# Optimization experiments

Hardware: AMD Instinct MI355X
Metric: run time of the kernel (lower is better)

The kernel has to match this reference:

```python
import jax, jax.numpy as jnp
import numpy as np

BETA = 0.95
THR = 1.0  # snntorch Leaky default threshold

# Heaviside spike with ATan surrogate gradient (snntorch default, alpha=2):
# d/dx = 1 / (1 + (pi*x)^2)
@jax.custom_vjp
def spike_fn(x):
    return (x > 0).astype(x.dtype)

def _spike_fwd(x):
    return spike_fn(x), x

def _spike_bwd(x, g):
    return (g / (1.0 + (jnp.pi * x) ** 2),)

spike_fn.defvjp(_spike_fwd, _spike_bwd)


def setup_inputs() -> dict:
    key = jax.random.key(0)
    ks = jax.random.split(key, 5)
    T, B, D_in, D_h, D_out = 25, 4096, 784, 1000, 10
    x = jax.random.normal(ks[0], (T, B, D_in), dtype=jnp.float32)
    # Kaiming-uniform-ish init like nn.Linear
    w1 = jax.random.uniform(ks[1], (D_h, D_in), jnp.float32, -1, 1) / np.sqrt(D_in)
    b1 = jax.random.uniform(ks[2], (D_h,), jnp.float32, -1, 1) / np.sqrt(D_in)
    w2 = jax.random.uniform(ks[3], (D_out, D_h), jnp.float32, -1, 1) / np.sqrt(D_h)
    b2 = jax.random.uniform(ks[4], (D_out,), jnp.float32, -1, 1) / np.sqrt(D_h)
    return {"x": x, "w1": w1, "b1": b1, "w2": w2, "b2": b2}


def reference(x, w1, b1, w2, b2):
    B = x.shape[1]
    mem1_0 = jnp.zeros((B, w1.shape[0]), x.dtype)
    mem2_0 = jnp.zeros((B, w2.shape[0]), x.dtype)

    def step(carry, xt):
        mem1, mem2 = carry
        # layer 1: Linear + Leaky (reset-by-subtraction, reset from prior mem)
        cur1 = xt @ w1.T + b1
        reset1 = spike_fn(mem1 - THR)
        mem1 = BETA * mem1 + cur1 - reset1 * THR
        spk1 = spike_fn(mem1 - THR)
        # layer 2
        cur2 = spk1 @ w2.T + b2
        reset2 = spike_fn(mem2 - THR)
        mem2 = BETA * mem2 + cur2 - reset2 * THR
        spk2 = spike_fn(mem2 - THR)
        return (mem1, mem2), spk2

    (mem1, mem2), spk_rec = jax.lax.scan(step, (mem1_0, mem2_0), x)
    return spk_rec, mem2
```

## Files before the change

### kernel.cpp

```cpp
#include <hip/hip_runtime.h>

typedef _Float16 f16;
typedef _Float16 f16x4 __attribute__((ext_vector_type(4)));
typedef _Float16 f16x8 __attribute__((ext_vector_type(8)));
typedef float f32x4 __attribute__((ext_vector_type(4)));

#define T_STEPS 25
#define BATCH   4096
#define DIN     784
#define DH      1000
#define HP      1024
#define DOUT    10
#define MROWS   (T_STEPS * BATCH)
#define KSEG    800
#define KA      (2 * KSEG)
#define KB      (3 * KSEG)
#define NTILES  (KB / 32)

__global__ void aconv_kernel(const float* __restrict__ x, f16* __restrict__ Ah)
{
    const int total = MROWS * 200;
    for (int idx = blockIdx.x * blockDim.x + threadIdx.x; idx < total;
         idx += gridDim.x * blockDim.x) {
        const int r  = idx / 200;
        const int c4 = (idx - r * 200) * 4;
        f16x4 hi, lo;
        if (c4 < DIN) {
            const float4 v = *(const float4*)(x + (size_t)r * DIN + c4);
            const float vv[4] = {v.x, v.y, v.z, v.w};
            #pragma unroll
            for (int j = 0; j < 4; ++j) {
                f16 h = (f16)vv[j];
                hi[j] = h;
                lo[j] = (f16)(vv[j] - (float)h);
            }
        } else {
            #pragma unroll
            for (int j = 0; j < 4; ++j) { hi[j] = (f16)0.f; lo[j] = (f16)0.f; }
        }
        *(f16x4*)(Ah + (size_t)r * KA + c4)        = hi;
        *(f16x4*)(Ah + (size_t)r * KA + KSEG + c4) = lo;
    }
}

__global__ void wconv_kernel(const float* __restrict__ w1, const float* __restrict__ b1,
                             const float* __restrict__ w2,
                             f16* __restrict__ Wh, float* __restrict__ b1p,
                             float* __restrict__ w2t)
{
    const int stride = gridDim.x * blockDim.x;
    const int tid0 = blockIdx.x * blockDim.x + threadIdx.x;
    for (int idx = tid0; idx < HP * KB; idx += stride) {
        const int n  = idx / KB;
        const int k  = idx - n * KB;
        const int seg = k / KSEG;
        const int kc  = k - seg * KSEG;
        float w = (n < DH && kc < DIN) ? w1[n * DIN + kc] : 0.f;
        f16 h = (f16)w;
        Wh[idx] = (seg < 2) ? h : (f16)(w - (float)h);
    }
    for (int idx = tid0; idx < HP; idx += stride)
        b1p[idx] = (idx < DH) ? b1[idx] : 0.f;
    for (int idx = tid0; idx < HP * DOUT; idx += stride) {
        const int h = idx / DOUT;
        const int o = idx - h * DOUT;
        w2t[idx] = (h < DH) ? w2[o * DH + h] : 0.f;
    }
}

#define GL(gp, ldsoff) __builtin_amdgcn_global_load_lds( \
    (const __attribute__((address_space(1))) void*)(gp), \
    (__attribute__((address_space(3))) void*)(lds + (ldsoff)), 16, 0, 0)

#define STAGE_A(tt) do { \
    const int ak_ = (((tt) < 50) ? (tt) : ((tt) - 50)) * 32; \
    GL(Ag + ak_,            ((tt) & 3) * 8192 + widoff); \
    GL(Ag + ak_ + 128 * KA, ((tt) & 3) * 8192 + 4096 + widoff); } while (0)
#define STAGE_B(tt) do { \
    const int bk_ = (tt) * 32; \
    GL(Bg + bk_,                     32768 + ((tt) & 3) * 8192 + widoff); \
    GL(Bg + bk_ + (size_t)128 * KB,  32768 + ((tt) & 3) * 8192 + 4096 + widoff); } while (0)

#define MFMA16(M0) \
    acc[M0+0][0] = __builtin_amdgcn_mfma_f32_16x16x32_f16(af0, bf0, acc[M0+0][0], 0, 0, 0); \
    acc[M0+0][1] = __builtin_amdgcn_mfma_f32_16x16x32_f16(af0, bf1, acc[M0+0][1], 0, 0, 0); \
    acc[M0+0][2] = __builtin_amdgcn_mfma_f32_16x16x32_f16(af0, bf2, acc[M0+0][2], 0, 0, 0); \
    acc[M0+0][3] = __builtin_amdgcn_mfma_f32_16x16x32_f16(af0, bf3, acc[M0+0][3], 0, 0, 0); \
    acc[M0+1][0] = __builtin_amdgcn_mfma_f32_16x16x32_f16(af1, bf0, acc[M0+1][0], 0, 0, 0); \
    acc[M0+1][1] = __builtin_amdgcn_mfma_f32_16x16x32_f16(af1, bf1, acc[M0+1][1], 0, 0, 0); \
    acc[M0+1][2] = __builtin_amdgcn_mfma_f32_16x16x32_f16(af1, bf2, acc[M0+1][2], 0, 0, 0); \
    acc[M0+1][3] = __builtin_amdgcn_mfma_f32_16x16x32_f16(af1, bf3, acc[M0+1][3], 0, 0, 0); \
    acc[M0+2][0] = __builtin_amdgcn_mfma_f32_16x16x32_f16(af2, bf0, acc[M0+2][0], 0, 0, 0); \
    acc[M0+2][1] = __builtin_amdgcn_mfma_f32_16x16x32_f16(af2, bf1, acc[M0+2][1], 0, 0, 0); \
    acc[M0+2][2] = __builtin_amdgcn_mfma_f32_16x16x32_f16(af2, bf2, acc[M0+2][2], 0, 0, 0); \
    acc[M0+2][3] = __builtin_amdgcn_mfma_f32_16x16x32_f16(af2, bf3, acc[M0+2][3], 0, 0, 0); \
    acc[M0+3][0] = __builtin_amdgcn_mfma_f32_16x16x32_f16(af3, bf0, acc[M0+3][0], 0, 0, 0); \
    acc[M0+3][1] = __builtin_amdgcn_mfma_f32_16x16x32_f16(af3, bf1, acc[M0+3][1], 0, 0, 0); \
    acc[M0+3][2] = __builtin_amdgcn_mfma_f32_16x16x32_f16(af3, bf2, acc[M0+3][2], 0, 0, 0); \
    acc[M0+3][3] = __builtin_amdgcn_mfma_f32_16x16x32_f16(af3, bf3, acc[M0+3][3], 0, 0, 0);

#define BODY(tt, STG, WAITSTR) do { \
    const int bA = ((tt) & 3) * 8192; \
    const int bB = 32768 + ((tt) & 3) * 8192; \
    f16x8 af0, af1, af2, af3, bf0, bf1, bf2, bf3; \
     \
    af0 = *(const f16x8*)(lds + bA + aoffb + 0 * 512); \
    af1 = *(const f16x8*)(lds + bA + aoffb + 1 * 512); \
    af2 = *(const f16x8*)(lds + bA + aoffb + 2 * 512); \
    af3 = *(const f16x8*)(lds + bA + aoffb + 3 * 512); \
    bf0 = *(const f16x8*)(lds + bB + boffb + 0 * 512); \
    bf1 = *(const f16x8*)(lds + bB + boffb + 1 * 512); \
    bf2 = *(const f16x8*)(lds + bB + boffb + 2 * 512); \
    bf3 = *(const f16x8*)(lds + bB + boffb + 3 * 512); \
    if (STG) STAGE_A((tt) + 3); \
    __builtin_amdgcn_s_barrier(); \
    asm volatile("s_waitcnt lgkmcnt(0)" ::: "memory"); \
    __builtin_amdgcn_sched_barrier(0); \
    __builtin_amdgcn_s_setprio(1); \
    MFMA16(0) \
    __builtin_amdgcn_s_setprio(0); \
    __builtin_amdgcn_s_barrier(); \
     \
    af0 = *(const f16x8*)(lds + bA + aoffb + 4 * 512); \
    af1 = *(const f16x8*)(lds + bA + aoffb + 5 * 512); \
    af2 = *(const f16x8*)(lds + bA + aoffb + 6 * 512); \
    af3 = *(const f16x8*)(lds + bA + aoffb + 7 * 512); \
    if (STG) STAGE_B((tt) + 3); \
    asm volatile(WAITSTR ::: "memory"); \
    __builtin_amdgcn_s_barrier(); \
    asm volatile("s_waitcnt lgkmcnt(0)" ::: "memory"); \
    __builtin_amdgcn_sched_barrier(0); \
    __builtin_amdgcn_s_setprio(1); \
    MFMA16(4) \
    __builtin_amdgcn_s_setprio(0); \
    __builtin_amdgcn_s_barrier(); \
} while (0)

__global__ __launch_bounds__(512, 2)
void gemm_kernel(const f16* __restrict__ A, const f16* __restrict__ B,
                 const float* __restrict__ bias, float* __restrict__ C)
{
    __shared__ f16 lds[65536];

    const int bid = blockIdx.x;
    const int swz = (bid & 7) * 200 + (bid >> 3);
    const int mt = swz >> 2;
    const int nt = swz & 3;
    const size_t rowBase = (size_t)mt * 256;
    const int colBase = nt * 256;

    const int tid  = threadIdx.x;
    const int wid  = tid >> 6;
    const int lane = tid & 63;
    const int wm = wid >> 2;
    const int wn = wid & 3;

    const int srow = tid >> 2;
    const int g = (tid & 3) ^ ((tid >> 3) & 3);
    const f16* Ag = A + (rowBase + srow) * KA + g * 8;
    const f16* Bg = B + (size_t)(colBase + srow) * KB + g * 8;
    const int widoff = wid * 512;

    const int cq = (lane >> 4) ^ (((lane & 15) >> 1) & 3);
    const int aoffb = (wm * 128 + (lane & 15)) * 32 + cq * 8;
    const int boffb = (wn * 64  + (lane & 15)) * 32 + cq * 8;

    f32x4 acc[8][4];
    #pragma unroll
    for (int m = 0; m < 8; ++m)
        #pragma unroll
        for (int n = 0; n < 4; ++n)
            acc[m][n] = (f32x4){0.f, 0.f, 0.f, 0.f};

    STAGE_A(0 - 3 + 3); STAGE_B(0);
    STAGE_A(1);         STAGE_B(1);
    STAGE_A(2);         STAGE_B(2);
    asm volatile("s_waitcnt vmcnt(8)" ::: "memory");
    __builtin_amdgcn_s_barrier();

    #pragma unroll 4
    for (int t = 0; t < NTILES - 3; ++t)
        BODY(t, 1, "s_waitcnt vmcnt(8)");
    BODY(NTILES - 3, 0, "s_waitcnt vmcnt(4)");
    BODY(NTILES - 2, 0, "s_waitcnt vmcnt(0)");
    BODY(NTILES - 1, 0, "");

    const int c_col0 = colBase + wn * 64 + (lane & 15);
    const size_t c_row0 = rowBase + wm * 128 + (lane >> 4) * 4;
    #pragma unroll
    for (int n = 0; n < 4; ++n) {
        const int gcol = c_col0 + n * 16;
        const float bv = bias[gcol];
        #pragma unroll
        for (int m = 0; m < 8; ++m) {
            const size_t grow = c_row0 + m * 16;
            #pragma unroll
            for (int r = 0; r < 4; ++r)
                C[(grow + r) * HP + gcol] = acc[m][n][r] + bv;
        }
    }
}

__global__ __launch_bounds__(256)
void phase2_kernel(const float* __restrict__ cur1, const float* __restrict__ w2t,
                   const float* __restrict__ b2, float* __restrict__ out)
{
    __shared__ float w2s[HP * DOUT];
    const int tid = threadIdx.x;
    for (int i = tid; i < HP * DOUT; i += 256) w2s[i] = w2t[i];

    const int lane = tid & 63;
    const int wave = tid >> 6;
    const int b = blockIdx.x * 4 + wave;

    float m1[16];
    #pragma unroll
    for (int i = 0; i < 16; ++i) m1[i] = 0.f;
    float m2[DOUT], b2r[DOUT];
    #pragma unroll
    for (int o = 0; o < DOUT; ++o) { m2[o] = 0.f; b2r[o] = b2[o]; }
    __syncthreads();

    for (int t = 0; t < T_STEPS; ++t) {
        const float* cr = cur1 + ((size_t)t * BATCH + b) * HP;
        float p[DOUT];
        #pragma unroll
        for (int o = 0; o < DOUT; ++o) p[o] = 0.f;

        #pragma unroll
        for (int c = 0; c < 4; ++c) {
            const float4 cu = *(const float4*)(cr + c * 256 + lane * 4);
            const float cv[4] = {cu.x, cu.y, cu.z, cu.w};
            #pragma unroll
            for (int j = 0; j < 4; ++j) {
                const float mo = m1[c * 4 + j];
                const float rs = (mo > 1.0f) ? 1.0f : 0.0f;
                const float mn = 0.95f * mo + cv[j] - rs;
                m1[c * 4 + j] = mn;
                if (mn > 1.0f) {
                    const float* wr = w2s + (c * 256 + lane * 4 + j) * DOUT;
                    #pragma unroll
                    for (int o = 0; o < DOUT; ++o) p[o] += wr[o];
                }
            }
        }
        #pragma unroll
        for (int o = 0; o < DOUT; ++o) {
            float v = p[o];
            #pragma unroll
            for (int msk = 32; msk > 0; msk >>= 1) v += __shfl_xor(v, msk, 64);
            p[o] = v;
        }
        #pragma unroll
        for (int o = 0; o < DOUT; ++o) {
            const float cur2 = p[o] + b2r[o];
            const float mo = m2[o];
            const float rs = (mo > 1.0f) ? 1.0f : 0.0f;
            m2[o] = 0.95f * mo + cur2 - rs;
        }
        if (lane < DOUT)
            out[(size_t)t * (BATCH * DOUT) + (size_t)b * DOUT + lane] =
                (m2[lane] > 1.0f) ? 1.0f : 0.0f;
    }
    if (lane < DOUT)
        out[(size_t)T_STEPS * BATCH * DOUT + (size_t)b * DOUT + lane] = m2[lane];
}

extern "C" void kernel_launch(void* const* d_in, const int* in_sizes, int n_in,
                              void* d_out, int out_size, void* d_ws, size_t ws_size,
                              hipStream_t stream)
{
    const float* x  = (const float*)d_in[0];
    const float* w1 = (const float*)d_in[1];
    const float* b1 = (const float*)d_in[2];
    const float* w2 = (const float*)d_in[3];
    const float* b2 = (const float*)d_in[4];
    float* out = (float*)d_out;

    char* wsb = (char*)d_ws;
    f16*   Ah   = (f16*)(wsb);
    f16*   Wh   = (f16*)(wsb + 327680000);
    float* cur1 = (float*)(wsb + 327680000 + 4915200);
    float* b1p  = (float*)(wsb + 327680000 + 4915200 + 419430400);
    float* w2t  = (float*)(wsb + 327680000 + 4915200 + 419430400 + 4096);

    aconv_kernel<<<4096, 256, 0, stream>>>(x, Ah);
    wconv_kernel<<<1024, 256, 0, stream>>>(w1, b1, w2, Wh, b1p, w2t);
    gemm_kernel<<<1600, 512, 0, stream>>>(Ah, Wh, b1p, cur1);
    phase2_kernel<<<1024, 256, 0, stream>>>(cur1, w2t, b2, out);
}
```

Before: 764.2 us.

## Load all A fragments up front and cut GEMM tile barriers to one

The per-tile body of the fp16 MFMA GEMM now reads all eight A fragments and four B fragments from LDS at the start. It issues the A and B global-to-LDS prefetches together and uses lgkmcnt(4) so the first MFMA half can start while the second half's fragments are still arriving. Three of the four s_barriers per K-tile are removed, leaving one at the end. The loop unroll drops from 4 to 2. The aim is less synchronisation stall and more overlap of LDS reads with MFMA, at the cost of 16 extra live VGPRs per thread. Under the 512-thread, 2-block launch bound that could cause spills or lower occupancy.

```diff
diff --git a/kernel.cpp b/kernel.cpp
--- a/kernel.cpp
+++ b/kernel.cpp
@@ -81,29 +81,28 @@
     GL(Bg + bk_,                     32768 + ((tt) & 3) * 8192 + widoff); \
     GL(Bg + bk_ + (size_t)128 * KB,  32768 + ((tt) & 3) * 8192 + 4096 + widoff); } while (0)
 
-#define MFMA16(M0) \
-    acc[M0+0][0] = __builtin_amdgcn_mfma_f32_16x16x32_f16(af0, bf0, acc[M0+0][0], 0, 0, 0); \
-    acc[M0+0][1] = __builtin_amdgcn_mfma_f32_16x16x32_f16(af0, bf1, acc[M0+0][1], 0, 0, 0); \
-    acc[M0+0][2] = __builtin_amdgcn_mfma_f32_16x16x32_f16(af0, bf2, acc[M0+0][2], 0, 0, 0); \
-    acc[M0+0][3] = __builtin_amdgcn_mfma_f32_16x16x32_f16(af0, bf3, acc[M0+0][3], 0, 0, 0); \
-    acc[M0+1][0] = __builtin_amdgcn_mfma_f32_16x16x32_f16(af1, bf0, acc[M0+1][0], 0, 0, 0); \
-    acc[M0+1][1] = __builtin_amdgcn_mfma_f32_16x16x32_f16(af1, bf1, acc[M0+1][1], 0, 0, 0); \
-    acc[M0+1][2] = __builtin_amdgcn_mfma_f32_16x16x32_f16(af1, bf2, acc[M0+1][2], 0, 0, 0); \
-    acc[M0+1][3] = __builtin_amdgcn_mfma_f32_16x16x32_f16(af1, bf3, acc[M0+1][3], 0, 0, 0); \
-    acc[M0+2][0] = __builtin_amdgcn_mfma_f32_16x16x32_f16(af2, bf0, acc[M0+2][0], 0, 0, 0); \
-    acc[M0+2][1] = __builtin_amdgcn_mfma_f32_16x16x32_f16(af2, bf1, acc[M0+2][1], 0, 0, 0); \
-    acc[M0+2][2] = __builtin_amdgcn_mfma_f32_16x16x32_f16(af2, bf2, acc[M0+2][2], 0, 0, 0); \
-    acc[M0+2][3] = __builtin_amdgcn_mfma_f32_16x16x32_f16(af2, bf3, acc[M0+2][3], 0, 0, 0); \
-    acc[M0+3][0] = __builtin_amdgcn_mfma_f32_16x16x32_f16(af3, bf0, acc[M0+3][0], 0, 0, 0); \
-    acc[M0+3][1] = __builtin_amdgcn_mfma_f32_16x16x32_f16(af3, bf1, acc[M0+3][1], 0, 0, 0); \
-    acc[M0+3][2] = __builtin_amdgcn_mfma_f32_16x16x32_f16(af3, bf2, acc[M0+3][2], 0, 0, 0); \
-    acc[M0+3][3] = __builtin_amdgcn_mfma_f32_16x16x32_f16(af3, bf3, acc[M0+3][3], 0, 0, 0);
+#define MFMA16(A0, A1, A2, A3, M0) \
+    acc[M0+0][0] = __builtin_amdgcn_mfma_f32_16x16x32_f16(A0, bf0, acc[M0+0][0], 0, 0, 0); \
+    acc[M0+0][1] = __builtin_amdgcn_mfma_f32_16x16x32_f16(A0, bf1, acc[M0+0][1], 0, 0, 0); \
+    acc[M0+0][2] = __builtin_amdgcn_mfma_f32_16x16x32_f16(A0, bf2, acc[M0+0][2], 0, 0, 0); \
+    acc[M0+0][3] = __builtin_amdgcn_mfma_f32_16x16x32_f16(A0, bf3, acc[M0+0][3], 0, 0, 0); \
+    acc[M0+1][0] = __builtin_amdgcn_mfma_f32_16x16x32_f16(A1, bf0, acc[M0+1][0], 0, 0, 0); \
+    acc[M0+1][1] = __builtin_amdgcn_mfma_f32_16x16x32_f16(A1, bf1, acc[M0+1][1], 0, 0, 0); \
+    acc[M0+1][2] = __builtin_amdgcn_mfma_f32_16x16x32_f16(A1, bf2, acc[M0+1][2], 0, 0, 0); \
+    acc[M0+1][3] = __builtin_amdgcn_mfma_f32_16x16x32_f16(A1, bf3, acc[M0+1][3], 0, 0, 0); \
+    acc[M0+2][0] = __builtin_amdgcn_mfma_f32_16x16x32_f16(A2, bf0, acc[M0+2][0], 0, 0, 0); \
+    acc[M0+2][1] = __builtin_amdgcn_mfma_f32_16x16x32_f16(A2, bf1, acc[M0+2][1], 0, 0, 0); \
+    acc[M0+2][2] = __builtin_amdgcn_mfma_f32_16x16x32_f16(A2, bf2, acc[M0+2][2], 0, 0, 0); \
+    acc[M0+2][3] = __builtin_amdgcn_mfma_f32_16x16x32_f16(A2, bf3, acc[M0+2][3], 0, 0, 0); \
+    acc[M0+3][0] = __builtin_amdgcn_mfma_f32_16x16x32_f16(A3, bf0, acc[M0+3][0], 0, 0, 0); \
+    acc[M0+3][1] = __builtin_amdgcn_mfma_f32_16x16x32_f16(A3, bf1, acc[M0+3][1], 0, 0, 0); \
+    acc[M0+3][2] = __builtin_amdgcn_mfma_f32_16x16x32_f16(A3, bf2, acc[M0+3][2], 0, 0, 0); \
+    acc[M0+3][3] = __builtin_amdgcn_mfma_f32_16x16x32_f16(A3, bf3, acc[M0+3][3], 0, 0, 0);
 
 #define BODY(tt, STG, WAITSTR) do { \
     const int bA = ((tt) & 3) * 8192; \
     const int bB = 32768 + ((tt) & 3) * 8192; \
-    f16x8 af0, af1, af2, af3, bf0, bf1, bf2, bf3; \
-     \
+    f16x8 af0, af1, af2, af3, af4, af5, af6, af7, bf0, bf1, bf2, bf3; \
     af0 = *(const f16x8*)(lds + bA + aoffb + 0 * 512); \
     af1 = *(const f16x8*)(lds + bA + aoffb + 1 * 512); \
     af2 = *(const f16x8*)(lds + bA + aoffb + 2 * 512); \
@@ -112,27 +111,24 @@
     bf1 = *(const f16x8*)(lds + bB + boffb + 1 * 512); \
     bf2 = *(const f16x8*)(lds + bB + boffb + 2 * 512); \
     bf3 = *(const f16x8*)(lds + bB + boffb + 3 * 512); \
-    if (STG) STAGE_A((tt) + 3); \
-    __builtin_amdgcn_s_barrier(); \
+    __builtin_amdgcn_sched_barrier(0); \
+    af4 = *(const f16x8*)(lds + bA + aoffb + 4 * 512); \
+    af5 = *(const f16x8*)(lds + bA + aoffb + 5 * 512); \
+    af6 = *(const f16x8*)(lds + bA + aoffb + 6 * 512); \
+    af7 = *(const f16x8*)(lds + bA + aoffb + 7 * 512); \
+    __builtin_amdgcn_sched_barrier(0); \
+    if (STG) { STAGE_A((tt) + 3); STAGE_B((tt) + 3); } \
+    asm volatile("s_waitcnt lgkmcnt(4)" ::: "memory"); \
+    __builtin_amdgcn_sched_barrier(0); \
+    __builtin_amdgcn_s_setprio(1); \
+    MFMA16(af0, af1, af2, af3, 0) \
+    __builtin_amdgcn_s_setprio(0); \
     asm volatile("s_waitcnt lgkmcnt(0)" ::: "memory"); \
     __builtin_amdgcn_sched_barrier(0); \
     __builtin_amdgcn_s_setprio(1); \
-    MFMA16(0) \
+    MFMA16(af4, af5, af6, af7, 4) \
     __builtin_amdgcn_s_setprio(0); \
-    __builtin_amdgcn_s_barrier(); \
-     \
-    af0 = *(const f16x8*)(lds + bA + aoffb + 4 * 512); \
-    af1 = *(const f16x8*)(lds + bA + aoffb + 5 * 512); \
-    af2 = *(const f16x8*)(lds + bA + aoffb + 6 * 512); \
-    af3 = *(const f16x8*)(lds + bA + aoffb + 7 * 512); \
-    if (STG) STAGE_B((tt) + 3); \
     asm volatile(WAITSTR ::: "memory"); \
-    __builtin_amdgcn_s_barrier(); \
-    asm volatile("s_waitcnt lgkmcnt(0)" ::: "memory"); \
-    __builtin_amdgcn_sched_barrier(0); \
-    __builtin_amdgcn_s_setprio(1); \
-    MFMA16(4) \
-    __builtin_amdgcn_s_setprio(0); \
     __builtin_amdgcn_s_barrier(); \
 } while (0)
 
@@ -172,13 +168,13 @@
         for (int n = 0; n < 4; ++n)
             acc[m][n] = (f32x4){0.f, 0.f, 0.f, 0.f};
 
-    STAGE_A(0 - 3 + 3); STAGE_B(0);
-    STAGE_A(1);         STAGE_B(1);
-    STAGE_A(2);         STAGE_B(2);
+    STAGE_A(0); STAGE_B(0);
+    STAGE_A(1); STAGE_B(1);
+    STAGE_A(2); STAGE_B(2);
     asm volatile("s_waitcnt vmcnt(8)" ::: "memory");
     __builtin_amdgcn_s_barrier();
 
-    #pragma unroll 4
+    #pragma unroll 2
     for (int t = 0; t < NTILES - 3; ++t)
         BODY(t, 1, "s_waitcnt vmcnt(8)");
     BODY(NTILES - 3, 0, "s_waitcnt vmcnt(4)");
```

New measurement: 778.2 us. About the same (+1.8%).
